# Performance work log

Hardware: AMD Instinct MI355X
Metric: run time of the kernel (lower is better)

The kernel has to match this reference:

```python
import jax, jax.numpy as jnp
import numpy as np

DIM = 128      # matrix dimension of the positional maps
N = 1024       # number of unique tree positions
MAX_POS = 65536  # positions < 2^16 -> path length <= 15 bits
L = 16         # static number of scan steps (covers max path length)


def setup_inputs() -> dict:
    key = jax.random.key(0)
    k1, k2 = jax.random.split(key)
    # replicate torch init: rand(2,d,d).softmax(-1).cumsum(-1)
    u = jax.random.uniform(k1, (2, DIM, DIM), dtype=jnp.float32)
    primitives = jnp.cumsum(jax.nn.softmax(u, axis=-1), axis=-1)
    unique = jax.random.randint(k2, (N,), 0, MAX_POS, dtype=jnp.int64)
    return {"unique": unique, "primitives": primitives}


def reference(unique, primitives):
    dtype = primitives.dtype
    dim = primitives.shape[-1]
    # hermitian = P - P^H (real -> skew-symmetric); primitives = matrix_exp(hermitian)
    herm = primitives - jnp.swapaxes(primitives, -1, -2)          # [2, d, d]
    expP = jax.vmap(jax.scipy.linalg.expm)(herm)                  # [2, d, d]
    eye = jnp.eye(dim, dtype=dtype)
    # linear(x, W) = x @ W.T ; word==2 (padding / exhausted path) applies identity
    trans = jnp.stack([expP[0].T, expP[1].T, eye])                # [3, d, d]

    # pos_to_path: bits of pos, LSB-first, dropping the leading 1.
    # bit at step s is (pos >> s) & 1, valid while (pos >> s) >= 2; pos<=1 -> empty path.
    steps = jnp.arange(L, dtype=unique.dtype)
    shifted = unique[None, :] >> steps[:, None]                   # [L, N]
    words = jnp.where(shifted >= 2, shifted & 1, 2)               # [L, N] in {0,1,2}

    def step(maps, w):
        # maps[n] <- maps[n] @ trans[w[n]]   (sequential composition along the path)
        return jnp.einsum('nij,njk->nik', maps, trans[w]), None

    maps0 = jnp.broadcast_to(eye, (unique.shape[0], dim, dim))    # identity.repeat(N,1,1)
    maps, _ = jax.lax.scan(step, maps0, words)
    return maps
```

## Files before the change

### kernel.cpp

```cpp
#include <hip/hip_runtime.h>

typedef unsigned int uint32;
typedef unsigned short u16;
typedef __attribute__((ext_vector_type(8))) short bf16x8;
typedef __attribute__((ext_vector_type(4))) float f32x4;
typedef __attribute__((ext_vector_type(2))) uint32 u32x2;
typedef __attribute__((ext_vector_type(4))) uint32 u32x4;

#define DIM 128
#define MAT (DIM * DIM)
#define GR  2048
#define PLANE 16384
#define MFMA __builtin_amdgcn_mfma_f32_16x16x32_bf16


__device__ __forceinline__ u16 f2bf(float x) {
    uint32 u = __float_as_uint(x);
    u += 0x7fffu + ((u >> 16) & 1u);
    return (u16)(u >> 16);
}
__device__ __forceinline__ float bf2f(u16 h) { return __uint_as_float(((uint32)h) << 16); }
__device__ __forceinline__ void split2(float x, u16& a0, u16& a1) {
    a0 = f2bf(x); a1 = f2bf(x - bf2f(a0));
}
__device__ __forceinline__ uint32 pack2(u16 a, u16 b) { return (uint32)a | ((uint32)b << 16); }
__device__ __forceinline__ uint4 packu4(const u16 (&a)[8]) {
    uint4 v; v.x = pack2(a[0], a[1]); v.y = pack2(a[2], a[3]);
    v.z = pack2(a[4], a[5]); v.w = pack2(a[6], a[7]); return v;
}
__device__ __forceinline__ uint32 comp4(const uint4& v, int c) {
    return c == 0 ? v.x : c == 1 ? v.y : c == 2 ? v.z : v.w;
}
__device__ __forceinline__ void transp8(const uint4 (&in)[8], uint4 (&out)[8]) {
#pragma unroll
    for (int c = 0; c < 8; ++c) {
        u16 o[8];
#pragma unroll
        for (int k = 0; k < 8; ++k) o[k] = (u16)(comp4(in[k], c >> 1) >> ((c & 1) * 16));
        out[c].x = pack2(o[0], o[1]); out[c].y = pack2(o[2], o[3]);
        out[c].z = pack2(o[4], o[5]); out[c].w = pack2(o[6], o[7]);
    }
}

template<bool PBLDS, int NP>
__device__ __forceinline__ void mm2(const uint4* __restrict__ pah, const uint4* __restrict__ pal,
                                    const uint4* __restrict__ pbh, const uint4* __restrict__ pbl,
                                    f32x4 (&acc)[4][4]) {
    const int tid = threadIdx.x, lane = tid & 63, w = tid >> 6;
    const int wr = (w >> 1) * 64, wc = (w & 1) * 64, lr = lane & 15, lg = lane >> 4;
#pragma unroll 1
    for (int kb = 0; kb < 4; ++kb) {
        const int g = kb * 4 + lg;
        bf16x8 ah[4], al[4], bh[4], bl[4];
#pragma unroll
        for (int t = 0; t < 4; ++t) {
            int ra = wr + t * 16 + lr;
            ah[t] = *(const bf16x8*)&pah[g * 128 + ra];
            if (NP == 3) al[t] = *(const bf16x8*)&pal[g * 128 + ra];
            int rb = wc + t * 16 + lr;
            int ib = PBLDS ? (rb * 16 + (g ^ (rb & 7))) : (g * 128 + rb);
            bh[t] = *(const bf16x8*)&pbh[ib];
            if (NP == 3) bl[t] = *(const bf16x8*)&pbl[ib];
        }
#pragma unroll
        for (int i = 0; i < 4; ++i)
#pragma unroll
            for (int j = 0; j < 4; ++j) {
                acc[i][j] = MFMA(ah[i], bh[j], acc[i][j], 0, 0, 0);
                if (NP == 3) {
                    acc[i][j] = MFMA(ah[i], bl[j], acc[i][j], 0, 0, 0);
                    acc[i][j] = MFMA(al[i], bh[j], acc[i][j], 0, 0, 0);
                }
            }
    }
}

__device__ __forceinline__ void acc_to_lds2(const f32x4 (&acc)[4][4], uint4* Mh, uint4* Ml) {
    const int tid = threadIdx.x, lane = tid & 63, w = tid >> 6;
    const int wr = (w >> 1) * 64, wc = (w & 1) * 64, lr = lane & 15, lg = lane >> 4;
#pragma unroll
    for (int i = 0; i < 4; ++i) {
        int u0 = wr + i * 16 + 4 * lg, half = (u0 >> 2) & 1, gq = u0 >> 3;
#pragma unroll
        for (int j = 0; j < 4; ++j) {
            int m = wc + j * 16 + lr;
            u16 h[4], l[4];
#pragma unroll
            for (int q = 0; q < 4; ++q) split2(acc[i][j][q], h[q], l[q]);
            uint2 hv; hv.x = pack2(h[0], h[1]); hv.y = pack2(h[2], h[3]);
            uint2 lv; lv.x = pack2(l[0], l[1]); lv.y = pack2(l[2], l[3]);
            int base = m * 16 + (gq ^ (m & 7));
            ((uint2*)&Mh[base])[half] = hv;
            ((uint2*)&Ml[base])[half] = lv;
        }
    }
}

__device__ __forceinline__ void acc_to_gN(const f32x4 (&acc)[4][4], uint4* nh, uint4* nl) {
    const int tid = threadIdx.x, lane = tid & 63, w = tid >> 6;
    const int wr = (w >> 1) * 64, wc = (w & 1) * 64, lr = lane & 15, lg = lane >> 4;
#pragma unroll
    for (int i = 0; i < 4; ++i) {
        int u0 = wr + i * 16 + 4 * lg, half = (u0 >> 2) & 1, gq = u0 >> 3;
#pragma unroll
        for (int j = 0; j < 4; ++j) {
            int m = wc + j * 16 + lr;
            u16 h[4], l[4];
#pragma unroll
            for (int q = 0; q < 4; ++q) split2(acc[i][j][q], h[q], l[q]);
            uint2 hv; hv.x = pack2(h[0], h[1]); hv.y = pack2(h[2], h[3]);
            uint2 lv; lv.x = pack2(l[0], l[1]); lv.y = pack2(l[2], l[3]);
            int base = gq * 128 + m;
            ((uint2*)&nh[base])[half] = hv;
            ((uint2*)&nl[base])[half] = lv;
        }
    }
}
__device__ __forceinline__ void acc_to_gN1(const f32x4 (&acc)[4][4], uint4* nh) {
    const int tid = threadIdx.x, lane = tid & 63, w = tid >> 6;
    const int wr = (w >> 1) * 64, wc = (w & 1) * 64, lr = lane & 15, lg = lane >> 4;
#pragma unroll
    for (int i = 0; i < 4; ++i) {
        int u0 = wr + i * 16 + 4 * lg, half = (u0 >> 2) & 1, gq = u0 >> 3;
#pragma unroll
        for (int j = 0; j < 4; ++j) {
            int m = wc + j * 16 + lr;
            u16 h[4];
#pragma unroll
            for (int q = 0; q < 4; ++q) h[q] = f2bf(acc[i][j][q]);
            uint2 hv; hv.x = pack2(h[0], h[1]); hv.y = pack2(h[2], h[3]);
            ((uint2*)&nh[gq * 128 + m])[half] = hv;
        }
    }
}

__device__ __forceinline__ void acc_to_out(const f32x4 (&acc)[4][4], float* O) {
    const int tid = threadIdx.x, lane = tid & 63, w = tid >> 6;
    const int wr = (w >> 1) * 64, wc = (w & 1) * 64, lr = lane & 15, lg = lane >> 4;
#pragma unroll
    for (int i = 0; i < 4; ++i) {
        int u0 = wr + i * 16 + 4 * lg;
#pragma unroll
        for (int j = 0; j < 4; ++j) {
            int m = wc + j * 16 + lr;
            *(f32x4*)&O[m * DIM + u0] = acc[i][j];
        }
    }
}

__device__ __forceinline__ void mm2w(const uint4* __restrict__ pah, const uint4* __restrict__ pal,
                                     const uint4* __restrict__ pbh, const uint4* __restrict__ pbl,
                                     f32x4 (&acc)[2][2]) {
    const int tid = threadIdx.x, lane = tid & 63, w = tid >> 6;
    const int wr = (w >> 2) * 32, wc = (w & 3) * 32, lr = lane & 15, lg = lane >> 4;
#pragma unroll 1
    for (int kb = 0; kb < 4; ++kb) {
        const int g = kb * 4 + lg;
        bf16x8 ah[2], al[2], bh[2], bl[2];
#pragma unroll
        for (int t = 0; t < 2; ++t) {
            int ra = wr + t * 16 + lr;
            ah[t] = *(const bf16x8*)&pah[g * 128 + ra];
            al[t] = *(const bf16x8*)&pal[g * 128 + ra];
            int rb = wc + t * 16 + lr;
            int ib = rb * 16 + (g ^ (rb & 7));
            bh[t] = *(const bf16x8*)&pbh[ib];
            bl[t] = *(const bf16x8*)&pbl[ib];
        }
#pragma unroll
        for (int i = 0; i < 2; ++i)
#pragma unroll
            for (int j = 0; j < 2; ++j) {
                acc[i][j] = MFMA(ah[i], bh[j], acc[i][j], 0, 0, 0);
                acc[i][j] = MFMA(ah[i], bl[j], acc[i][j], 0, 0, 0);
                acc[i][j] = MFMA(al[i], bh[j], acc[i][j], 0, 0, 0);
            }
    }
}
__device__ __forceinline__ void acc_to_lds2w(const f32x4 (&acc)[2][2], uint4* Mh, uint4* Ml) {
    const int tid = threadIdx.x, lane = tid & 63, w = tid >> 6;
    const int wr = (w >> 2) * 32, wc = (w & 3) * 32, lr = lane & 15, lg = lane >> 4;
#pragma unroll
    for (int i = 0; i < 2; ++i) {
        int u0 = wr + i * 16 + 4 * lg, half = (u0 >> 2) & 1, gq = u0 >> 3;
#pragma unroll
        for (int j = 0; j < 2; ++j) {
            int m = wc + j * 16 + lr;
            u16 h[4], l[4];
#pragma unroll
            for (int q = 0; q < 4; ++q) split2(acc[i][j][q], h[q], l[q]);
            uint2 hv; hv.x = pack2(h[0], h[1]); hv.y = pack2(h[2], h[3]);
            uint2 lv; lv.x = pack2(l[0], l[1]); lv.y = pack2(l[2], l[3]);
            int base = m * 16 + (gq ^ (m & 7));
            ((uint2*)&Mh[base])[half] = hv;
            ((uint2*)&Ml[base])[half] = lv;
        }
    }
}

__device__ __forceinline__ void stage_lds(const uint4* sh, const uint4* sl, uint4* Mh, uint4* Ml) {
    for (int s = threadIdx.x; s < GR; s += blockDim.x) {
        int g = s >> 7, row = s & 127;
        int d = row * 16 + (g ^ (row & 7));
        Mh[d] = sh[s]; Ml[d] = sl[s];
    }
}
__device__ __forceinline__ void copyN(const uint4* Mh, const uint4* Ml, uint4* dh, uint4* dl) {
    for (int s2 = threadIdx.x; s2 < 2 * GR; s2 += blockDim.x) {
        const uint4* src = (s2 & GR) ? Ml : Mh;
        uint4* dst = (s2 & GR) ? dl : dh;
        int s = s2 & (GR - 1);
        int g = s >> 7, row = s & 127;
        dst[s] = src[row * 16 + (g ^ (row & 7))];
    }
}
__device__ __forceinline__ void copyT(const uint4* Mh, const uint4* Ml, uint4* dh, uint4* dl) {
    for (int tk = threadIdx.x; tk < 512; tk += blockDim.x) {
        const uint4* src = (tk & 256) ? Ml : Mh;
        uint4* dst = (tk & 256) ? dl : dh;
        int t = tk & 255, br = t >> 4, bc = t & 15;
        uint4 in[8], out[8];
#pragma unroll
        for (int k = 0; k < 8; ++k) { int r = br * 8 + k; in[k] = src[r * 16 + (bc ^ (r & 7))]; }
        transp8(in, out);
#pragma unroll
        for (int k = 0; k < 8; ++k) dst[br * 128 + bc * 8 + k] = out[k];
    }
}


__device__ __forceinline__ void wlds2s(u16* dst, int m, int u0, f32x4 v) {
    u16 a0[4], a1[4];
#pragma unroll
    for (int q = 0; q < 4; ++q) split2(v[q], a0[q], a1[q]);
    int e = ((m >> 2) * 8 + (u0 >> 4)) * 64 + (m & 3) * 16 + (u0 & 15);
    uint2 w0; w0.x = pack2(a0[0], a0[1]); w0.y = pack2(a0[2], a0[3]);
    uint2 w1; w1.x = pack2(a1[0], a1[1]); w1.y = pack2(a1[2], a1[3]);
    *(uint2*)&dst[0 * PLANE + e] = w0;
    *(uint2*)&dst[1 * PLANE + e] = w1;
}

template<bool ATR>
__device__ __forceinline__ void mmS(const uint4* __restrict__ pa, const u16* __restrict__ XSu,
                                    f32x4 (&acc)[2][4], int wr, int wc, int lr, int lg) {
#pragma unroll
    for (int i = 0; i < 2; ++i)
#pragma unroll
        for (int j = 0; j < 4; ++j) { f32x4 z = {0.f, 0.f, 0.f, 0.f}; acc[i][j] = z; }
    const uint32 lds_base = (uint32)(size_t)(const void*)XSu;
#pragma unroll 1
    for (int kb = 0; kb < 4; ++kb) {
        const int g = kb * 4 + lg;
        u32x2 t0[2][2], t1[2][2];
        bf16x8 aa[2][2], bb[4][2];
        if (ATR) {
#pragma unroll
            for (int t = 0; t < 2; ++t) {
                uint32 ba = lds_base + (uint32)(((16 * g + (wr >> 4) + t) << 7) + 8 * lr);
#pragma unroll
                for (int sp = 0; sp < 2; ++sp) {
                    asm volatile("ds_read_b64_tr_b16 %0, %2\n\t"
                                 "ds_read_b64_tr_b16 %1, %2 offset:1024"
                                 : "=&v"(t0[t][sp]), "=&v"(t1[t][sp])
                                 : "v"(ba + (uint32)(sp * 2 * PLANE)));
                }
            }
        } else {
#pragma unroll
            for (int t = 0; t < 2; ++t) {
                int ra = wr + t * 16 + lr;
#pragma unroll
                for (int sp = 0; sp < 2; ++sp) aa[t][sp] = *(const bf16x8*)&pa[sp * GR + g * 128 + ra];
            }
        }
#pragma unroll
        for (int t = 0; t < 4; ++t) {
            int rb = wc + t * 16 + lr;
            int e = ((rb >> 2) * 8 + (g >> 1)) * 64 + (rb & 3) * 16 + (g & 1) * 8;
#pragma unroll
            for (int sp = 0; sp < 2; ++sp) bb[t][sp] = *(const bf16x8*)&XSu[sp * PLANE + e];
        }
        if (ATR) {
            asm volatile("s_waitcnt lgkmcnt(0)" ::: "memory");
            __builtin_amdgcn_sched_barrier(0);
#pragma unroll
            for (int t = 0; t < 2; ++t)
#pragma unroll
                for (int sp = 0; sp < 2; ++sp) {
                    u32x4 v; v.x = t0[t][sp].x; v.y = t0[t][sp].y;
                    v.z = t1[t][sp].x; v.w = t1[t][sp].y;
                    aa[t][sp] = *(bf16x8*)&v;
                }
        }
#pragma unroll
        for (int i = 0; i < 2; ++i)
#pragma unroll
            for (int j = 0; j < 4; ++j) {
                acc[i][j] = MFMA(aa[i][0], bb[j][0], acc[i][j], 0, 0, 0);
                acc[i][j] = MFMA(aa[i][0], bb[j][1], acc[i][j], 0, 0, 0);
                acc[i][j] = MFMA(aa[i][1], bb[j][0], acc[i][j], 0, 0, 0);
            }
    }
}

__global__ __launch_bounds__(512) void expm_kernel(
        const float* __restrict__ P, float* __restrict__ NBf, float* __restrict__ NB2f,
        u16* TBp, u16* TB3p,
        u16* TThp, u16* TTlp, u16* TNhp, u16* TNlp) {
    __shared__ uint4 XL[4 * GR];
    u16* XSu = (u16*)XL;
    u16* PR0 = XSu;
    u16* PR1 = XSu + 2 * PLANE;
    const int b = blockIdx.x, tid = threadIdx.x;
    const int lane = tid & 63, w = tid >> 6;
    const int wr = (w >> 1) * 32, wc = (w & 1) * 64, lr = lane & 15, lg = lane >> 4;
    const float* Pm = P + b * MAT;
    float* nbf = NBf + b * MAT;
    float* nb2f = NB2f + b * MAT;
    uint4* tb  = (uint4*)TBp  + (size_t)b * 3 * GR;
    uint4* tb3 = (uint4*)TB3p + (size_t)b * 3 * GR;
    uint4* TTh = (uint4*)TThp; uint4* TTl = (uint4*)TTlp;
    uint4* TNh = (uint4*)TNhp; uint4* TNl = (uint4*)TNlp;

    const float C6f = 1.0f / 720.0f, C7f = 1.0f / 5040.0f, C8f = 1.0f / 40320.0f, C9f = 1.0f / 362880.0f;

    for (int s = tid; s < GR; s += 512) {
        int r = s >> 4, g = s & 15;
        float vv[8];
#pragma unroll
        for (int k = 0; k < 8; ++k) {
            int c = g * 8 + k;
            vv[k] = (Pm[r * DIM + c] - Pm[c * DIM + r]) * (1.0f / 32.0f);
        }
        float4 f0; f0.x = vv[0]; f0.y = vv[1]; f0.z = vv[2]; f0.w = vv[3];
        float4 f1; f1.x = vv[4]; f1.y = vv[5]; f1.z = vv[6]; f1.w = vv[7];
        *(float4*)&nbf[r * DIM + g * 8] = f0;
        *(float4*)&nbf[r * DIM + g * 8 + 4] = f1;
        u16 s0[8], s1[8];
#pragma unroll
        for (int k = 0; k < 8; ++k) split2(vv[k], s0[k], s1[k]);
        int d = ((r >> 2) * 8 + (g >> 1)) * 64 + (r & 3) * 16 + (g & 1) * 8;
        *(uint4*)&PR0[0 * PLANE + d] = packu4(s0);
        *(uint4*)&PR0[1 * PLANE + d] = packu4(s1);
#pragma unroll
        for (int k = 0; k < 8; ++k) { s0[k] ^= 0x8000; s1[k] ^= 0x8000; }
        int gi = g * 128 + r;
        tb[0 * GR + gi] = packu4(s0); tb[1 * GR + gi] = packu4(s1);
    }
    __syncthreads();

    f32x4 acc[2][4];

    mmS<true>(nullptr, PR0, acc, wr, wc, lr, lg);
#pragma unroll
    for (int i = 0; i < 2; ++i) { int u0 = wr + i * 16 + 4 * lg;
#pragma unroll
        for (int j = 0; j < 4; ++j) { int m = wc + j * 16 + lr;
            *(f32x4*)&nb2f[m * DIM + u0] = acc[i][j];
            wlds2s(PR1, m, u0, acc[i][j]);
        } }
    __syncthreads();

    mmS<false>(tb, PR1, acc, wr, wc, lr, lg);
#pragma unroll
    for (int i = 0; i < 2; ++i) { int u0 = wr + i * 16 + 4 * lg; int half = (u0 >> 2) & 1; int gi = (u0 >> 3) * 128;
#pragma unroll
        for (int j = 0; j < 4; ++j) { int m = wc + j * 16 + lr;
            f32x4 a = acc[i][j];
            u16 a0[4], a1[4];
#pragma unroll
            for (int q = 0; q < 4; ++q) split2(-a[q], a0[q], a1[q]);
            uint2 w0; w0.x = pack2(a0[0], a0[1]); w0.y = pack2(a0[2], a0[3]);
            uint2 w1; w1.x = pack2(a1[0], a1[1]); w1.y = pack2(a1[2], a1[3]);
            ((uint2*)&tb3[0 * GR + gi + m])[half] = w0;
            ((uint2*)&tb3[1 * GR + gi + m])[half] = w1;
            f32x4 bv = *(const f32x4*)&nbf[m * DIM + u0];
            f32x4 b2v = *(const f32x4*)&nb2f[m * DIM + u0];
            f32x4 x0;
#pragma unroll
            for (int q = 0; q < 4; ++q)
                x0[q] = a[q] * C9f + b2v[q] * C8f + bv[q] * C7f + ((u0 + q == m) ? C6f : 0.0f);
            wlds2s(PR0, m, u0, x0);
        } }
    __syncthreads();

    mmS<false>(tb3, PR0, acc, wr, wc, lr, lg);
#pragma unroll
    for (int i = 0; i < 2; ++i) { int u0 = wr + i * 16 + 4 * lg;
#pragma unroll
        for (int j = 0; j < 4; ++j) { int m = wc + j * 16 + lr;
            f32x4 bv = *(const f32x4*)&nbf[m * DIM + u0];
            f32x4 b2v = *(const f32x4*)&nb2f[m * DIM + u0];
            f32x4 x1;
#pragma unroll
            for (int q = 0; q < 4; ++q)
                x1[q] = acc[i][j][q] + bv[q] * (1.0f / 24.0f) + b2v[q] * (1.0f / 120.0f)
                      + ((u0 + q == m) ? (1.0f / 6.0f) : 0.0f);
            wlds2s(PR1, m, u0, x1);
        } }
    __syncthreads();

    mmS<false>(tb3, PR1, acc, wr, wc, lr, lg);
#pragma unroll
    for (int i = 0; i < 2; ++i) { int u0 = wr + i * 16 + 4 * lg;
#pragma unroll
        for (int j = 0; j < 4; ++j) { int m = wc + j * 16 + lr;
            f32x4 bv = *(const f32x4*)&nbf[m * DIM + u0];
            f32x4 b2v = *(const f32x4*)&nb2f[m * DIM + u0];
            f32x4 x2;
#pragma unroll
            for (int q = 0; q < 4; ++q)
                x2[q] = acc[i][j][q] + bv[q] + b2v[q] * 0.5f + ((u0 + q == m) ? 1.0f : 0.0f);
            wlds2s(PR0, m, u0, x2);
        } }
    __syncthreads();

    for (int sq = 0; sq < 5; ++sq) {
        const u16* src = (sq & 1) ? PR1 : PR0;
        u16* dst = (sq & 1) ? PR0 : PR1;
        mmS<true>(nullptr, src, acc, wr, wc, lr, lg);
        if (sq < 4) {
#pragma unroll
            for (int i = 0; i < 2; ++i) { int u0 = wr + i * 16 + 4 * lg;
#pragma unroll
                for (int j = 0; j < 4; ++j) wlds2s(dst, wc + j * 16 + lr, u0, acc[i][j]);
            }
            __syncthreads();
        } else {
#pragma unroll
            for (int i = 0; i < 2; ++i) { int u0 = wr + i * 16 + 4 * lg; int half = (u0 >> 2) & 1;
#pragma unroll
                for (int j = 0; j < 4; ++j) { int m = wc + j * 16 + lr;
                    u16 h[4], l[4];
#pragma unroll
                    for (int q = 0; q < 4; ++q) split2(acc[i][j][q], h[q], l[q]);
                    uint2 hv; hv.x = pack2(h[0], h[1]); hv.y = pack2(h[2], h[3]);
                    uint2 lv; lv.x = pack2(l[0], l[1]); lv.y = pack2(l[2], l[3]);
                    int base = m * 16 + ((u0 >> 3) ^ (m & 7));
                    ((uint2*)&XL[2 * GR + base])[half] = hv;
                    ((uint2*)&XL[3 * GR + base])[half] = lv;
                } }
            __syncthreads();
            copyN(XL + 2 * GR, XL + 3 * GR, TTh + (size_t)b * GR, TTl + (size_t)b * GR);
            copyT(XL + 2 * GR, XL + 3 * GR, TNh + (size_t)b * GR, TNl + (size_t)b * GR);
        }
    }
}

__device__ __forceinline__ uint4* nv4h_p(u16* XTgp, u16* TBp, int i) {
    return i < 3 ? (uint4*)XTgp + (size_t)(2 * i) * GR : (uint4*)TBp + (size_t)2 * GR;
}
__device__ __forceinline__ uint4* nv4l_p(u16* XTgp, u16* TBp, int i) {
    return i < 3 ? (uint4*)XTgp + (size_t)(2 * i + 1) * GR : (uint4*)TBp + (size_t)5 * GR;
}

__global__ __launch_bounds__(256) void levelA_kernel(u16* TThp, u16* TTlp, u16* TNhp, u16* TNlp,
                                                     u16* XTgp, u16* TBp) {
    uint4* TTh = (uint4*)TThp; uint4* TTl = (uint4*)TTlp;
    uint4* TNh = (uint4*)TNhp; uint4* TNl = (uint4*)TNlp;
    int b = blockIdx.x;
    if (b == 8) {
        for (int s = threadIdx.x; s < GR; s += 256) {
            int g = s >> 7, row = s & 127;
            u16 h[8];
#pragma unroll
            for (int k = 0; k < 8; ++k) h[k] = (g * 8 + k == row) ? (u16)0x3F80 : (u16)0;
            TNh[(size_t)274 * GR + s] = packu4(h);
            uint4 z; z.x = z.y = z.z = z.w = 0u;
            TNl[(size_t)274 * GR + s] = z;
        }
        return;
    }
    int c = 4 + (b & 3);
    int b0 = c & 1, b1 = (c >> 1) & 1;
    f32x4 acc[4][4] = {};
    if (b < 4) {
        mm2<false, 3>(TNh + (size_t)b0 * GR, TNl + (size_t)b0 * GR,
                      TTh + (size_t)b1 * GR, TTl + (size_t)b1 * GR, acc);
        acc_to_gN(acc, TTh + (size_t)(c - 2) * GR, TTl + (size_t)(c - 2) * GR);
    } else {
        mm2<false, 3>(TTh + (size_t)b1 * GR, TTl + (size_t)b1 * GR,
                      TNh + (size_t)b0 * GR, TNl + (size_t)b0 * GR, acc);
        acc_to_gN(acc, nv4h_p(XTgp, TBp, b - 4), nv4l_p(XTgp, TBp, b - 4));
    }
}

__global__ __launch_bounds__(256) void levelB_kernel(u16* TThp, u16* TTlp, u16* TNhp, u16* TNlp,
                                                     u16* XTgp, u16* TBp) {
    uint4* TTh = (uint4*)TThp; uint4* TTl = (uint4*)TTlp;
    uint4* TNh = (uint4*)TNhp; uint4* TNl = (uint4*)TNlp;
    int b = blockIdx.x;
    f32x4 acc[4][4] = {};
    if (b < 8) {
        int i = b;
        mm2<false, 3>(TNh + (size_t)(i & 1) * GR, TNl + (size_t)(i & 1) * GR,
                      TTh + (size_t)(2 + (i >> 1)) * GR, TTl + (size_t)(2 + (i >> 1)) * GR, acc);
        acc_to_gN(acc, TTh + (size_t)(6 + i) * GR, TTl + (size_t)(6 + i) * GR);
    } else if (b < 24) {
        int i = b - 8;
        mm2<false, 3>(nv4h_p(XTgp, TBp, i & 3), nv4l_p(XTgp, TBp, i & 3),
                      TTh + (size_t)(2 + (i >> 2)) * GR, TTl + (size_t)(2 + (i >> 2)) * GR, acc);
        acc_to_gN(acc, TTh + (size_t)(14 + i) * GR, TTl + (size_t)(14 + i) * GR);
    } else {
        int i = b - 24;
        mm2<false, 3>(TTh + (size_t)(2 + (i >> 2)) * GR, TTl + (size_t)(2 + (i >> 2)) * GR,
                      nv4h_p(XTgp, TBp, i & 3), nv4l_p(XTgp, TBp, i & 3), acc);
        acc_to_gN(acc, TNh + (size_t)(2 + i) * GR, TNl + (size_t)(2 + i) * GR);
    }
}

__global__ __launch_bounds__(1024) void chain_kernel(u16* TThp, u16* TTlp, u16* TNhp, u16* TNlp,
                                                     int schemeA) {
    __shared__ uint4 Mh[GR], Ml[GR];
    uint4* TTh = (uint4*)TThp; uint4* TTl = (uint4*)TTlp;
    uint4* TNh = (uint4*)TNhp; uint4* TNl = (uint4*)TNlp;
    int b = blockIdx.x;
    if (b == 28) {
        int id = schemeA ? 274 : 126;
        for (int s = threadIdx.x; s < GR; s += 1024) {
            int g = s >> 7, row = s & 127;
            u16 h[8];
#pragma unroll
            for (int k = 0; k < 8; ++k) h[k] = (g * 8 + k == row) ? (u16)0x3F80 : (u16)0;
            TNh[(size_t)id * GR + s] = packu4(h);
            uint4 z; z.x = z.y = z.z = z.w = 0u;
            TNl[(size_t)id * GR + s] = z;
        }
        return;
    }
    int v = 4 + b;
    int nb = 31 - __clz(v);
    int b0 = v & 1;
    stage_lds(TNh + (size_t)b0 * GR, TNl + (size_t)b0 * GR, Mh, Ml);
    __syncthreads();
    for (int t = 1; t < nb; ++t) {
        int bt = (v >> t) & 1;
        f32x4 acc[2][2] = {};
        mm2w(TTh + (size_t)bt * GR, TTl + (size_t)bt * GR, Mh, Ml, acc);
        __syncthreads();
        acc_to_lds2w(acc, Mh, Ml);
        __syncthreads();
    }
    copyT(Mh, Ml, TTh + (size_t)(v - 2) * GR, TTl + (size_t)(v - 2) * GR);
    bool needN = schemeA ? (v >= 16) : true;
    if (needN) {
        int tn = schemeA ? (v - 14) : (v - 2);
        copyN(Mh, Ml, TNh + (size_t)tn * GR, TNl + (size_t)tn * GR);
    }
}

__global__ __launch_bounds__(256) void pair_kernel(u16* TThp, u16* TTlp, u16* TNhp, u16* TNlp,
                                                   int schemeA) {
    extern __shared__ uint4 PL[];
    uint4* TTh = (uint4*)TThp; uint4* TTl = (uint4*)TTlp;
    uint4* TNh = (uint4*)TNhp; uint4* TNl = (uint4*)TNlp;
    int v = 32 + blockIdx.x;
    int c4 = v & 15;
    int tnb = schemeA ? (2 + c4) : (14 + c4);
    int tta = (v >> 4) - 2;
    if (schemeA) {
        f32x4 acc[4][4] = {};
        if (v < 256) {
            mm2<false, 3>(TNh + (size_t)tnb * GR, TNl + (size_t)tnb * GR,
                          TTh + (size_t)tta * GR, TTl + (size_t)tta * GR, acc);
            acc_to_gN1(acc, TTh + (size_t)(v - 2) * GR);
        } else {
            mm2<false, 3>(TTh + (size_t)tta * GR, TTl + (size_t)tta * GR,
                          TNh + (size_t)tnb * GR, TNl + (size_t)tnb * GR, acc);
            acc_to_gN1(acc, TNh + (size_t)(18 + (v - 256)) * GR);
        }
    } else {
        f32x4 acc[4][4] = {};
        mm2<false, 3>(TTh + (size_t)tta * GR, TTl + (size_t)tta * GR,
                      TNh + (size_t)tnb * GR, TNl + (size_t)tnb * GR, acc);
        acc_to_gN(acc, TNh + (size_t)(v - 2) * GR, TNl + (size_t)(v - 2) * GR);
        acc_to_lds2(acc, PL, PL + GR);
        __syncthreads();
        copyT(PL, PL + GR, TTh + (size_t)(v - 2) * GR, TTl + (size_t)(v - 2) * GR);
    }
}

__global__ __launch_bounds__(256) void final_kernel(const u16* TThp, const u16* TTlp,
                                                    const u16* TNhp, const u16* TNlp,
                                                    const int* __restrict__ uq,
                                                    float* __restrict__ out, int schemeA) {
    extern __shared__ uint4 FL[];
    const uint4* TTh = (const uint4*)TThp; const uint4* TTl = (const uint4*)TTlp;
    const uint4* TNh = (const uint4*)TNhp; const uint4* TNl = (const uint4*)TNlp;
    float* O = out + (size_t)blockIdx.x * MAT;
    unsigned p = (unsigned)uq[blockIdx.x];

    if (p < 2u) {
        for (int s = threadIdx.x; s < 4096; s += 256) {
            int r = s >> 5, c0 = (s & 31) * 4;
            float4 v; v.x = v.y = v.z = v.w = 0.f;
            int d = r - c0;
            if (d == 0) v.x = 1.f; else if (d == 1) v.y = 1.f;
            else if (d == 2) v.z = 1.f; else if (d == 3) v.w = 1.f;
            *(float4*)&O[r * DIM + c0] = v;
        }
        return;
    }

    const uint4 *pah, *pal, *pbh, *pbl;
    int m3 = -1;
    if (schemeA) {
        const int id = 274;
        if (p < 256u) {
            pah = TTh + (size_t)(p - 2) * GR; pal = TTl + (size_t)(p - 2) * GR;
            pbh = TNh + (size_t)id * GR;      pbl = TNl + (size_t)id * GR;
        } else {
            int lo = (int)(p & 255u); unsigned hi = p >> 8;
            pbh = TNh + (size_t)(18 + lo) * GR; pbl = TNl + (size_t)(18 + lo) * GR;
            if (hi >= 2u) { pah = TTh + (size_t)(hi - 2) * GR; pal = TTl + (size_t)(hi - 2) * GR; }
            else          { pah = TNh + (size_t)id * GR;       pal = TNl + (size_t)id * GR; }
        }
        f32x4 acc[4][4] = {};
        mm2<false, 1>(pah, pal, pbh, pbl, acc);
        acc_to_out(acc, O);
        return;
    }
    {
        int f[3]; int m = 0; unsigned q = p;
        while (q >= 128u) { f[m++] = 64 + (int)(q & 63u); q >>= 6; }
        f[m++] = (int)q;
        if (m == 1) {
            const uint4* sh = TNh + (size_t)(f[0] - 2) * GR;
            const uint4* sl = TNl + (size_t)(f[0] - 2) * GR;
            for (int s = threadIdx.x; s < GR; s += 256) {
                int row = s >> 4, g = s & 15;
                uint4 H = sh[g * 128 + row], L = sl[g * 128 + row];
                float4 o0, o1;
                o0.x = bf2f((u16)(H.x & 0xffff)) + bf2f((u16)(L.x & 0xffff));
                o0.y = bf2f((u16)(H.x >> 16))    + bf2f((u16)(L.x >> 16));
                o0.z = bf2f((u16)(H.y & 0xffff)) + bf2f((u16)(L.y & 0xffff));
                o0.w = bf2f((u16)(H.y >> 16))    + bf2f((u16)(L.y >> 16));
                o1.x = bf2f((u16)(H.z & 0xffff)) + bf2f((u16)(L.z & 0xffff));
                o1.y = bf2f((u16)(H.z >> 16))    + bf2f((u16)(L.z >> 16));
                o1.z = bf2f((u16)(H.w & 0xffff)) + bf2f((u16)(L.w & 0xffff));
                o1.w = bf2f((u16)(H.w >> 16))    + bf2f((u16)(L.w >> 16));
                *(float4*)&O[row * DIM + g * 8] = o0;
                *(float4*)&O[row * DIM + g * 8 + 4] = o1;
            }
            return;
        }
        pbh = TNh + (size_t)(f[0] - 2) * GR; pbl = TNl + (size_t)(f[0] - 2) * GR;
        pah = TTh + (size_t)(f[1] - 2) * GR; pal = TTl + (size_t)(f[1] - 2) * GR;
        if (m == 3) m3 = f[2] - 2;
    }

    f32x4 acc[4][4] = {};
    mm2<false, 3>(pah, pal, pbh, pbl, acc);
    if (m3 < 0) { acc_to_out(acc, O); return; }
    acc_to_lds2(acc, FL, FL + GR);
    __syncthreads();
    f32x4 a2[4][4] = {};
    mm2<true, 3>(TTh + (size_t)m3 * GR, TTl + (size_t)m3 * GR, FL, FL + GR, a2);
    acc_to_out(a2, O);
}

extern "C" void kernel_launch(void* const* d_in, const int* in_sizes, int n_in,
                              void* d_out, int out_size, void* d_ws, size_t ws_size,
                              hipStream_t stream) {
    const int*   uq = (const int*)d_in[0];
    const float* P  = (const float*)d_in[1];
    float* out = (float*)d_out;

    const size_t needA = (size_t)(2 * 254 + 2 * 275 + 18) * MAT * 2 + (size_t)4 * MAT * 4;
    const bool A = ws_size >= needA;
    const int nTT = A ? 254 : 126;
    const int nTN = A ? 275 : 127;

    u16* TTh = (u16*)d_ws;
    u16* TTl = TTh + (size_t)nTT * MAT;
    u16* TNh = TTl + (size_t)nTT * MAT;
    u16* TNl = TNh + (size_t)nTN * MAT;
    u16* TB  = TNl + (size_t)nTN * MAT;
    u16* TB3 = TB  + (size_t)6 * MAT;
    u16* XTg = TB3 + (size_t)6 * MAT;
    float* NBf  = (float*)(XTg + (size_t)6 * MAT);
    float* NB2f = NBf + 2 * MAT;

    expm_kernel<<<2, 512, 0, stream>>>(P, NBf, NB2f, TB, TB3, TTh, TTl, TNh, TNl);
    if (A) {
        levelA_kernel<<<9, 256, 0, stream>>>(TTh, TTl, TNh, TNl, XTg, TB);
        levelB_kernel<<<40, 256, 0, stream>>>(TTh, TTl, TNh, TNl, XTg, TB);
    } else {
        chain_kernel<<<29, 1024, 0, stream>>>(TTh, TTl, TNh, TNl, 0);
    }
    pair_kernel<<<A ? 480 : 96, 256, A ? 0 : 65536, stream>>>(TTh, TTl, TNh, TNl, (int)A);
    final_kernel<<<1024, 256, A ? 0 : 65536, stream>>>(TTh, TTl, TNh, TNl, uq, out, (int)A);
}
```

Measured before the change: 103.5 us.

## Fuse tree levels and pair stage into one kernel with atomic flag barriers

Result: slower. 142.2 us (+37.4%).

```diff
diff --git a/kernel.cpp b/kernel.cpp
--- a/kernel.cpp
+++ b/kernel.cpp
@@ -306,7 +306,7 @@
 __global__ __launch_bounds__(512) void expm_kernel(
         const float* __restrict__ P, float* __restrict__ NBf, float* __restrict__ NB2f,
         u16* TBp, u16* TB3p,
-        u16* TThp, u16* TTlp, u16* TNhp, u16* TNlp) {
+        u16* TThp, u16* TTlp, u16* TNhp, u16* TNlp, uint32* flags) {
     __shared__ uint4 XL[4 * GR];
     u16* XSu = (u16*)XL;
     u16* PR0 = XSu;
@@ -314,6 +314,7 @@
     const int b = blockIdx.x, tid = threadIdx.x;
     const int lane = tid & 63, w = tid >> 6;
     const int wr = (w >> 1) * 32, wc = (w & 1) * 64, lr = lane & 15, lg = lane >> 4;
+    if (b == 0 && tid == 0) { flags[0] = 0u; flags[1] = 0u; }
     const float* Pm = P + b * MAT;
     float* nbf = NBf + b * MAT;
     float* nb2f = NB2f + b * MAT;
@@ -428,7 +429,7 @@
             __syncthreads();
         } else {
 #pragma unroll
-            for (int i = 0; i < 2; ++i) { int u0 = wr + i * 16 + 4 * lg; int half = (u0 >> 2) & 1;
+            for (int i = 0; i < 2; ++i) { int u0 = wr + i * 16 + 4 * lg; int half = (u0 >> 2) & 1; int gq = u0 >> 3;
 #pragma unroll
                 for (int j = 0; j < 4; ++j) { int m = wc + j * 16 + lr;
                     u16 h[4], l[4];
@@ -436,12 +437,13 @@
                     for (int q = 0; q < 4; ++q) split2(acc[i][j][q], h[q], l[q]);
                     uint2 hv; hv.x = pack2(h[0], h[1]); hv.y = pack2(h[2], h[3]);
                     uint2 lv; lv.x = pack2(l[0], l[1]); lv.y = pack2(l[2], l[3]);
-                    int base = m * 16 + ((u0 >> 3) ^ (m & 7));
+                    ((uint2*)&TTh[(size_t)b * GR + gq * 128 + m])[half] = hv;
+                    ((uint2*)&TTl[(size_t)b * GR + gq * 128 + m])[half] = lv;
+                    int base = m * 16 + (gq ^ (m & 7));
                     ((uint2*)&XL[2 * GR + base])[half] = hv;
                     ((uint2*)&XL[3 * GR + base])[half] = lv;
                 } }
             __syncthreads();
-            copyN(XL + 2 * GR, XL + 3 * GR, TTh + (size_t)b * GR, TTl + (size_t)b * GR);
             copyT(XL + 2 * GR, XL + 3 * GR, TNh + (size_t)b * GR, TNl + (size_t)b * GR);
         }
     }
@@ -454,58 +456,87 @@
     return i < 3 ? (uint4*)XTgp + (size_t)(2 * i + 1) * GR : (uint4*)TBp + (size_t)5 * GR;
 }
 
-__global__ __launch_bounds__(256) void levelA_kernel(u16* TThp, u16* TTlp, u16* TNhp, u16* TNlp,
-                                                     u16* XTgp, u16* TBp) {
+__global__ __launch_bounds__(256) void tree_kernel(u16* TThp, u16* TTlp, u16* TNhp, u16* TNlp,
+                                                   u16* XTgp, u16* TBp, uint32* flags) {
     uint4* TTh = (uint4*)TThp; uint4* TTl = (uint4*)TTlp;
     uint4* TNh = (uint4*)TNhp; uint4* TNl = (uint4*)TNlp;
     int b = blockIdx.x;
-    if (b == 8) {
-        for (int s = threadIdx.x; s < GR; s += 256) {
-            int g = s >> 7, row = s & 127;
-            u16 h[8];
-#pragma unroll
-            for (int k = 0; k < 8; ++k) h[k] = (g * 8 + k == row) ? (u16)0x3F80 : (u16)0;
-            TNh[(size_t)274 * GR + s] = packu4(h);
-            uint4 z; z.x = z.y = z.z = z.w = 0u;
-            TNl[(size_t)274 * GR + s] = z;
-        }
+    if (b < 9) {
+        if (b == 8) {
+            for (int s = threadIdx.x; s < GR; s += 256) {
+                int g = s >> 7, row = s & 127;
+                u16 h[8];
+#pragma unroll
+                for (int k = 0; k < 8; ++k) h[k] = (g * 8 + k == row) ? (u16)0x3F80 : (u16)0;
+                TNh[(size_t)274 * GR + s] = packu4(h);
+                uint4 z; z.x = z.y = z.z = z.w = 0u;
+                TNl[(size_t)274 * GR + s] = z;
+            }
+            return;
+        }
+        int c = 4 + (b & 3);
+        int b0 = c & 1, b1 = (c >> 1) & 1;
+        f32x4 acc[4][4] = {};
+        if (b < 4) {
+            mm2<false, 3>(TNh + (size_t)b0 * GR, TNl + (size_t)b0 * GR,
+                          TTh + (size_t)b1 * GR, TTl + (size_t)b1 * GR, acc);
+            acc_to_gN(acc, TTh + (size_t)(c - 2) * GR, TTl + (size_t)(c - 2) * GR);
+        } else {
+            mm2<false, 3>(TTh + (size_t)b1 * GR, TTl + (size_t)b1 * GR,
+                          TNh + (size_t)b0 * GR, TNl + (size_t)b0 * GR, acc);
+            acc_to_gN(acc, nv4h_p(XTgp, TBp, b - 4), nv4l_p(XTgp, TBp, b - 4));
+        }
+        __syncthreads();
+        __threadfence();
+        if (threadIdx.x == 0) atomicAdd(&flags[0], 1u);
         return;
     }
-    int c = 4 + (b & 3);
-    int b0 = c & 1, b1 = (c >> 1) & 1;
+    if (b < 49) {
+        if (threadIdx.x == 0) {
+            while (atomicAdd(&flags[0], 0u) < 8u) __builtin_amdgcn_s_sleep(8);
+        }
+        __syncthreads();
+        __threadfence();
+        int i = b - 9;
+        f32x4 acc[4][4] = {};
+        if (i < 8) {
+            mm2<false, 3>(TNh + (size_t)(i & 1) * GR, TNl + (size_t)(i & 1) * GR,
+                          TTh + (size_t)(2 + (i >> 1)) * GR, TTl + (size_t)(2 + (i >> 1)) * GR, acc);
+            acc_to_gN(acc, TTh + (size_t)(6 + i) * GR, TTl + (size_t)(6 + i) * GR);
+        } else if (i < 24) {
+            int k = i - 8;
+            mm2<false, 3>(nv4h_p(XTgp, TBp, k & 3), nv4l_p(XTgp, TBp, k & 3),
+                          TTh + (size_t)(2 + (k >> 2)) * GR, TTl + (size_t)(2 + (k >> 2)) * GR, acc);
+            acc_to_gN(acc, TTh + (size_t)(14 + k) * GR, TTl + (size_t)(14 + k) * GR);
+        } else {
+            int k = i - 24;
+            mm2<false, 3>(TTh + (size_t)(2 + (k >> 2)) * GR, TTl + (size_t)(2 + (k >> 2)) * GR,
+                          nv4h_p(XTgp, TBp, k & 3), nv4l_p(XTgp, TBp, k & 3), acc);
+            acc_to_gN(acc, TNh + (size_t)(2 + k) * GR, TNl + (size_t)(2 + k) * GR);
+        }
+        __syncthreads();
+        __threadfence();
+        if (threadIdx.x == 0) atomicAdd(&flags[1], 1u);
+        return;
+    }
+    if (threadIdx.x == 0) {
+        while (atomicAdd(&flags[1], 0u) < 40u) __builtin_amdgcn_s_sleep(8);
+    }
+    __syncthreads();
+    __threadfence();
+    int v = 32 + (b - 49);
+    int c4 = v & 15;
+    int tnb = 2 + c4;
+    int tta = (v >> 4) - 2;
     f32x4 acc[4][4] = {};
-    if (b < 4) {
-        mm2<false, 3>(TNh + (size_t)b0 * GR, TNl + (size_t)b0 * GR,
-                      TTh + (size_t)b1 * GR, TTl + (size_t)b1 * GR, acc);
-        acc_to_gN(acc, TTh + (size_t)(c - 2) * GR, TTl + (size_t)(c - 2) * GR);
+    if (v < 256) {
+        mm2<false, 3>(TNh + (size_t)tnb * GR, TNl + (size_t)tnb * GR,
+                      TTh + (size_t)tta * GR, TTl + (size_t)tta * GR, acc);
+        acc_to_gN1(acc, TTh + (size_t)(v - 2) * GR);
     } else {
-        mm2<false, 3>(TTh + (size_t)b1 * GR, TTl + (size_t)b1 * GR,
-                      TNh + (size_t)b0 * GR, TNl + (size_t)b0 * GR, acc);
-        acc_to_gN(acc, nv4h_p(XTgp, TBp, b - 4), nv4l_p(XTgp, TBp, b - 4));
-    }
-}
-
-__global__ __launch_bounds__(256) void levelB_kernel(u16* TThp, u16* TTlp, u16* TNhp, u16* TNlp,
-                                                     u16* XTgp, u16* TBp) {
-    uint4* TTh = (uint4*)TThp; uint4* TTl = (uint4*)TTlp;
-    uint4* TNh = (uint4*)TNhp; uint4* TNl = (uint4*)TNlp;
-    int b = blockIdx.x;
-    f32x4 acc[4][4] = {};
-    if (b < 8) {
-        int i = b;
-        mm2<false, 3>(TNh + (size_t)(i & 1) * GR, TNl + (size_t)(i & 1) * GR,
-                      TTh + (size_t)(2 + (i >> 1)) * GR, TTl + (size_t)(2 + (i >> 1)) * GR, acc);
-        acc_to_gN(acc, TTh + (size_t)(6 + i) * GR, TTl + (size_t)(6 + i) * GR);
-    } else if (b < 24) {
-        int i = b - 8;
-        mm2<false, 3>(nv4h_p(XTgp, TBp, i & 3), nv4l_p(XTgp, TBp, i & 3),
-                      TTh + (size_t)(2 + (i >> 2)) * GR, TTl + (size_t)(2 + (i >> 2)) * GR, acc);
-        acc_to_gN(acc, TTh + (size_t)(14 + i) * GR, TTl + (size_t)(14 + i) * GR);
-    } else {
-        int i = b - 24;
-        mm2<false, 3>(TTh + (size_t)(2 + (i >> 2)) * GR, TTl + (size_t)(2 + (i >> 2)) * GR,
-                      nv4h_p(XTgp, TBp, i & 3), nv4l_p(XTgp, TBp, i & 3), acc);
-        acc_to_gN(acc, TNh + (size_t)(2 + i) * GR, TNl + (size_t)(2 + i) * GR);
+        mm2<false, 3>(TTh + (size_t)tta * GR, TTl + (size_t)tta * GR,
+                      TNh + (size_t)tnb * GR, TNl + (size_t)tnb * GR, acc);
+        acc_to_gN1(acc, TNh + (size_t)(18 + (v - 256)) * GR);
     }
 }
 
@@ -556,28 +587,15 @@
     uint4* TNh = (uint4*)TNhp; uint4* TNl = (uint4*)TNlp;
     int v = 32 + blockIdx.x;
     int c4 = v & 15;
-    int tnb = schemeA ? (2 + c4) : (14 + c4);
+    int tnb = 14 + c4;
     int tta = (v >> 4) - 2;
-    if (schemeA) {
-        f32x4 acc[4][4] = {};
-        if (v < 256) {
-            mm2<false, 3>(TNh + (size_t)tnb * GR, TNl + (size_t)tnb * GR,
-                          TTh + (size_t)tta * GR, TTl + (size_t)tta * GR, acc);
-            acc_to_gN1(acc, TTh + (size_t)(v - 2) * GR);
-        } else {
-            mm2<false, 3>(TTh + (size_t)tta * GR, TTl + (size_t)tta * GR,
-                          TNh + (size_t)tnb * GR, TNl + (size_t)tnb * GR, acc);
-            acc_to_gN1(acc, TNh + (size_t)(18 + (v - 256)) * GR);
-        }
-    } else {
-        f32x4 acc[4][4] = {};
-        mm2<false, 3>(TTh + (size_t)tta * GR, TTl + (size_t)tta * GR,
-                      TNh + (size_t)tnb * GR, TNl + (size_t)tnb * GR, acc);
-        acc_to_gN(acc, TNh + (size_t)(v - 2) * GR, TNl + (size_t)(v - 2) * GR);
-        acc_to_lds2(acc, PL, PL + GR);
-        __syncthreads();
-        copyT(PL, PL + GR, TTh + (size_t)(v - 2) * GR, TTl + (size_t)(v - 2) * GR);
-    }
+    f32x4 acc[4][4] = {};
+    mm2<false, 3>(TTh + (size_t)tta * GR, TTl + (size_t)tta * GR,
+                  TNh + (size_t)tnb * GR, TNl + (size_t)tnb * GR, acc);
+    acc_to_gN(acc, TNh + (size_t)(v - 2) * GR, TNl + (size_t)(v - 2) * GR);
+    acc_to_lds2(acc, PL, PL + GR);
+    __syncthreads();
+    copyT(PL, PL + GR, TTh + (size_t)(v - 2) * GR, TTl + (size_t)(v - 2) * GR);
 }
 
 __global__ __launch_bounds__(256) void final_kernel(const u16* TThp, const u16* TTlp,
@@ -680,14 +698,14 @@
     u16* XTg = TB3 + (size_t)6 * MAT;
     float* NBf  = (float*)(XTg + (size_t)6 * MAT);
     float* NB2f = NBf + 2 * MAT;
-
-    expm_kernel<<<2, 512, 0, stream>>>(P, NBf, NB2f, TB, TB3, TTh, TTl, TNh, TNl);
+    uint32* flags = (uint32*)(TB3 + (size_t)2 * MAT);
+
+    expm_kernel<<<2, 512, 0, stream>>>(P, NBf, NB2f, TB, TB3, TTh, TTl, TNh, TNl, flags);
     if (A) {
-        levelA_kernel<<<9, 256, 0, stream>>>(TTh, TTl, TNh, TNl, XTg, TB);
-        levelB_kernel<<<40, 256, 0, stream>>>(TTh, TTl, TNh, TNl, XTg, TB);
+        tree_kernel<<<529, 256, 0, stream>>>(TTh, TTl, TNh, TNl, XTg, TB, flags);
     } else {
         chain_kernel<<<29, 1024, 0, stream>>>(TTh, TTl, TNh, TNl, 0);
-    }
-    pair_kernel<<<A ? 480 : 96, 256, A ? 0 : 65536, stream>>>(TTh, TTl, TNh, TNl, (int)A);
+        pair_kernel<<<96, 256, 65536, stream>>>(TTh, TTl, TNh, TNl, 0);
+    }
     final_kernel<<<1024, 256, A ? 0 : 65536, stream>>>(TTh, TTl, TNh, TNl, uq, out, (int)A);
 }
```
